# Performance work log

Hardware: AMD Instinct MI355X
Metric: run time of the kernel (lower is better)

Reference implementation:

```python
import jax, jax.numpy as jnp
import numpy as np

N, M, E, B = 200000, 100000, 600000, 64
F_IN, H, EMB, V, NREL, NSRT = 256, 256, 128, 512, 4, 5


def setup_inputs() -> dict:
    key = jax.random.key(0)
    ks = jax.random.split(key, 24)
    s = 0.02
    inp = {
        "x": jax.random.normal(ks[0], (M, F_IN), jnp.float32),
        "x_batch": jnp.sort(jax.random.randint(ks[1], (M,), 0, B)),
        "tgt_y": jax.random.randint(ks[2], (N, 3), 0, V),
        "tgt_edge_index": jax.random.randint(ks[3], (2, E), 0, N),
        "tgt_edge_type": jax.random.randint(ks[4], (E,), 0, NREL),
        "tgt_y_batch": jnp.sort(jax.random.randint(ks[5], (N,), 0, B)),
        "embeds": jax.random.normal(ks[6], (V, EMB), jnp.float32) * s,
        "W_self1": jax.random.normal(ks[7], (EMB, H), jnp.float32) * s,
        "W_rel1": jax.random.normal(ks[8], (NREL, EMB, H), jnp.float32) * s,
        "W_ctx1": jax.random.normal(ks[9], (F_IN, H), jnp.float32) * s,
        "b1": jnp.zeros((H,), jnp.float32),
        "W_self2": jax.random.normal(ks[10], (H, H), jnp.float32) * s,
        "W_rel2": jax.random.normal(ks[11], (NREL, H, H), jnp.float32) * s,
        "W_ctx2": jax.random.normal(ks[12], (F_IN, H), jnp.float32) * s,
        "b2": jnp.zeros((H,), jnp.float32),
        "W_self3": jax.random.normal(ks[13], (H, EMB), jnp.float32) * s,
        "W_rel3": jax.random.normal(ks[14], (NREL, H, EMB), jnp.float32) * s,
        "W_ctx3": jax.random.normal(ks[15], (F_IN, EMB), jnp.float32) * s,
        "b3": jnp.zeros((EMB,), jnp.float32),
        "lin_z_w": jax.random.normal(ks[16], (EMB, V), jnp.float32) * s,
        "lin_z_b": jnp.zeros((V,), jnp.float32),
        "lin_g_w": jax.random.normal(ks[17], (2 * EMB, NSRT), jnp.float32) * s,
        "lin_g_b": jnp.zeros((NSRT,), jnp.float32),
    }
    return inp


def _gcn(x, x_batch, h, src, dst, etype, y_batch, Ws, Wr, Wc, b):
    # per-graph mean context from encoder nodes, gathered per decoder node
    cnt = jax.ops.segment_sum(jnp.ones((x.shape[0],), x.dtype), x_batch, num_segments=B)
    ctx = jax.ops.segment_sum(x, x_batch, num_segments=B) / jnp.maximum(cnt, 1.0)[:, None]
    hs = h[src]  # [E, d_in] gather
    msg = jnp.zeros((src.shape[0], Ws.shape[1]), h.dtype)
    for r in range(NREL):  # relation-typed messages (R-GCN style)
        msg = msg + jnp.where((etype == r)[:, None], hs @ Wr[r], 0.0)
    agg = jax.ops.segment_sum(msg, dst, num_segments=h.shape[0])  # scatter-add at dst
    return jax.nn.relu(h @ Ws + agg + ctx[y_batch] @ Wc + b)


def reference(x, x_batch, tgt_y, tgt_edge_index, tgt_edge_type, tgt_y_batch,
              embeds, W_self1, W_rel1, W_ctx1, b1, W_self2, W_rel2, W_ctx2, b2,
              W_self3, W_rel3, W_ctx3, b3, lin_z_w, lin_z_b, lin_g_w, lin_g_b):
    y = embeds[tgt_y].sum(axis=1)  # embedding gather-sum: [N, EMB]
    src, dst = tgt_edge_index[0], tgt_edge_index[1]
    y = _gcn(x, x_batch, y, src, dst, tgt_edge_type, tgt_y_batch, W_self1, W_rel1, W_ctx1, b1)
    y = _gcn(x, x_batch, y, src, dst, tgt_edge_type, tgt_y_batch, W_self2, W_rel2, W_ctx2, b2)
    y = _gcn(x, x_batch, y, src, dst, tgt_edge_type, tgt_y_batch, W_self3, W_rel3, W_ctx3, b3)
    y_pred = jax.nn.log_softmax(y @ lin_z_w + lin_z_b, axis=1)  # [N, V]
    # y[edge_index].permute(1,0,2).flatten(1) == concat(y[src], y[dst]) per edge
    ef = jnp.concatenate([y[src], y[dst]], axis=1)  # [E, 2*EMB]
    y_edge_pred = jax.nn.log_softmax(ef @ lin_g_w + lin_g_b, axis=1)  # [E, NSRT]
    return (y, tgt_edge_index, tgt_edge_type, y_pred, y_edge_pred)
```

## Files before the change

### kernel.cpp

```cpp
#include <hip/hip_runtime.h>
#include <hip/hip_bf16.h>
#include <stdint.h>

#define NN 200000
#define MM 100000
#define EE 600000
#define BB 64
#define F_IN 256
#define HH 256
#define EMB 128
#define VV 512
#define NSRT 5

typedef __attribute__((ext_vector_type(8))) short bf16x8;
typedef __attribute__((ext_vector_type(4))) float f32x4;

__device__ __forceinline__ unsigned short f2bf(float x){
    union { float f; unsigned int u; } c; c.f = x;
    unsigned int r = c.u + 0x7FFFu + ((c.u >> 16) & 1u);
    return (unsigned short)(r >> 16);
}
__device__ __forceinline__ float bf2f(unsigned short b){
    union { unsigned int u; float f; } c; c.u = ((unsigned int)b) << 16;
    return c.f;
}

__device__ __forceinline__ int lowerb(const int* a, int n, int key){
    int lo = 0, hi = n;
    while (lo < hi){ int mid = (lo + hi) >> 1; if (a[mid] < key) lo = mid + 1; else hi = mid; }
    return lo;
}

#define GLDS16(g, l) __builtin_amdgcn_global_load_lds( \
    (const __attribute__((address_space(1))) unsigned int*)(g), \
    (__attribute__((address_space(3))) unsigned int*)(l), 16, 0, 0)

#define CTX_RPB 128
__global__ __launch_bounds__(256) void ctxsum_kernel(const float* __restrict__ x,
        const int* __restrict__ xb, float* __restrict__ sum){
    int r0 = blockIdx.x * CTX_RPB;
    int r1 = r0 + CTX_RPB; if (r1 > MM) r1 = MM;
    int t = threadIdx.x;
    float s = 0.f;
    int g = xb[r0];
    for (int r = r0; r < r1; ++r){
        int gb = xb[r];
        if (gb != g){ atomicAdd(&sum[g * F_IN + t], s); s = 0.f; g = gb; }
        s += x[(size_t)r * F_IN + t];
    }
    atomicAdd(&sum[g * F_IN + t], s);
}

__global__ __launch_bounds__(256) void ctxdiv_kernel(const float* __restrict__ sum,
        const int* __restrict__ xb, float* __restrict__ ctx){
    int g = blockIdx.x, t = threadIdx.x;
    int lo = lowerb(xb, MM, g), hi = lowerb(xb, MM, g + 1);
    int c = hi - lo; if (c < 1) c = 1;
    ctx[g * F_IN + t] = sum[g * F_IN + t] / (float)c;
}

__global__ __launch_bounds__(64) void ctxb_kernel(const float* __restrict__ ctx,
        const float* __restrict__ Wc, const float* __restrict__ b,
        float* __restrict__ out, int dout){
    int g = blockIdx.x; int j = blockIdx.y * 64 + threadIdx.x;
    float acc = b[j];
    const float* cr = ctx + g * F_IN;
    for (int k = 0; k < F_IN; ++k) acc += cr[k] * Wc[(size_t)k * dout + j];
    out[(size_t)g * dout + j] = acc;
}

__global__ __launch_bounds__(256) void build_wt(const float* __restrict__ Ws,
        const float* __restrict__ Wr, unsigned short* __restrict__ WT,
        int din, int dout, int ktot){
    size_t idx = (size_t)blockIdx.x * 256 + threadIdx.x;
    size_t total = (size_t)dout * ktot;
    if (idx >= total) return;
    int j = (int)(idx / ktot), k = (int)(idx % ktot);
    float v = (k < din) ? Ws[(size_t)k * dout + j] : Wr[(size_t)(k - din) * dout + j];
    WT[idx] = f2bf(v);
}

__global__ __launch_bounds__(256) void build_wtp(const float* __restrict__ Ws,
        const float* __restrict__ Wr, unsigned short* __restrict__ WT,
        int K, int dout){
    size_t idx = (size_t)blockIdx.x * 256 + threadIdx.x;
    size_t total = (size_t)5 * dout * K;
    if (idx >= total) return;
    int jj = (int)(idx / K), k = (int)(idx % K);
    int blk = jj / dout, j = jj % dout;
    float v = (blk == 0) ? Ws[(size_t)k * dout + j]
                         : Wr[((size_t)(blk - 1) * K + k) * dout + j];
    WT[idx] = f2bf(v);
}

__global__ __launch_bounds__(256) void embed_kernel(const int* __restrict__ ty,
        const float* __restrict__ emb, unsigned short* __restrict__ h0){
    size_t idx = (size_t)blockIdx.x * 256 + threadIdx.x;
    int i = (int)(idx >> 7), c = (int)(idx & 127);
    int t0 = ty[i * 3], t1 = ty[i * 3 + 1], t2 = ty[i * 3 + 2];
    float v = emb[(size_t)t0 * EMB + c] + emb[(size_t)t1 * EMB + c] + emb[(size_t)t2 * EMB + c];
    h0[idx] = f2bf(v);
}

__global__ __launch_bounds__(256) void hist_kernel(const int* __restrict__ dst, int* __restrict__ deg){
    int e = blockIdx.x * 256 + threadIdx.x; if (e >= EE) return;
    atomicAdd(&deg[dst[e]], 1);
}

#define SNB ((NN + 1023) / 1024)

__global__ __launch_bounds__(256) void scanA_kernel(const int* __restrict__ deg,
        int* __restrict__ bsum){
    __shared__ int wsum[4];
    int tid = threadIdx.x, wid = tid >> 6, lane = tid & 63;
    int base = blockIdx.x * 1024 + tid * 4;
    int s = 0;
    if (base + 3 < NN){ int4 v = *(const int4*)(deg + base); s = v.x + v.y + v.z + v.w; }
    else { for (int i = 0; i < 4; ++i){ int idx = base + i; if (idx < NN) s += deg[idx]; } }
#pragma unroll
    for (int off = 1; off < 64; off <<= 1) s += __shfl_xor(s, off);
    if (lane == 0) wsum[wid] = s;
    __syncthreads();
    if (tid == 0) bsum[blockIdx.x] = wsum[0] + wsum[1] + wsum[2] + wsum[3];
}

__global__ __launch_bounds__(256) void scanB_kernel(const int* __restrict__ bsum,
        int* __restrict__ boff){
    __shared__ int lds[256];
    int t = threadIdx.x;
    int v = (t < SNB) ? bsum[t] : 0;
    lds[t] = v; __syncthreads();
    for (int off = 1; off < 256; off <<= 1){
        int n = (t >= off) ? lds[t - off] : 0;
        __syncthreads();
        lds[t] += n;
        __syncthreads();
    }
    if (t < SNB) boff[t] = lds[t] - v;
}

__global__ __launch_bounds__(256) void scanC_kernel(const int* __restrict__ deg,
        const int* __restrict__ boff, int* __restrict__ rowptr, int* __restrict__ cursor){
    __shared__ int wsum[4];
    int tid = threadIdx.x, wid = tid >> 6, lane = tid & 63;
    int base = blockIdx.x * 1024 + tid * 4;
    int d0 = 0, d1 = 0, d2 = 0, d3 = 0;
    if (base + 3 < NN){ int4 v = *(const int4*)(deg + base); d0 = v.x; d1 = v.y; d2 = v.z; d3 = v.w; }
    else if (base < NN){
        d0 = deg[base];
        if (base + 1 < NN) d1 = deg[base + 1];
        if (base + 2 < NN) d2 = deg[base + 2];
    }
    int tsum = d0 + d1 + d2 + d3;
    int run = tsum;
#pragma unroll
    for (int off = 1; off < 64; off <<= 1){
        int n = __shfl_up(run, off);
        if (lane >= off) run += n;
    }
    if (lane == 63) wsum[wid] = run;
    int texcl = run - tsum;
    __syncthreads();
    int woff = 0;
    for (int i = 0; i < wid; ++i) woff += wsum[i];
    int p = boff[blockIdx.x] + woff + texcl;
    if (base < NN){
        rowptr[base] = p; cursor[base] = p; p += d0;
        if (base + 1 < NN){ rowptr[base + 1] = p; cursor[base + 1] = p; p += d1; }
        if (base + 2 < NN){ rowptr[base + 2] = p; cursor[base + 2] = p; p += d2; }
        if (base + 3 < NN){ rowptr[base + 3] = p; cursor[base + 3] = p; p += d3; }
    }
    if (blockIdx.x == 0 && tid == 0) rowptr[NN] = EE;
}

__global__ __launch_bounds__(256) void fill_kernel(const int* __restrict__ src,
        const int* __restrict__ dst, const int* __restrict__ et,
        int* __restrict__ cursor, int* __restrict__ eidx){
    int e = blockIdx.x * 256 + threadIdx.x; if (e >= EE) return;
    int p = atomicAdd(&cursor[dst[e]], 1);
    eidx[p] = src[e] | (et[e] << 28);
}

template<int DIN>
__global__ __launch_bounds__(256) void sbuild_kernel(const unsigned short* __restrict__ h,
        const int* __restrict__ rowptr, const int* __restrict__ eidx,
        unsigned short* __restrict__ S){
    constexpr int CPL = DIN / 64;
    int wid = threadIdx.x >> 6, lane = threadIdx.x & 63;
    int d = blockIdx.x * 4 + wid;
    int lo = rowptr[d], hi = rowptr[d + 1];
    float acc0[CPL], acc1[CPL], acc2[CPL], acc3[CPL];
#pragma unroll
    for (int c = 0; c < CPL; ++c){ acc0[c] = 0.f; acc1[c] = 0.f; acc2[c] = 0.f; acc3[c] = 0.f; }
    const unsigned short* hl = h + lane * CPL;
    int e = lo;
    for (; e + 1 < hi; e += 2){
        int pkA = eidx[e], pkB = eidx[e + 1];
        int sA = pkA & 0x0FFFFFFF, rA = pkA >> 28;
        int sB = pkB & 0x0FFFFFFF, rB = pkB >> 28;
        unsigned short vA[CPL], vB[CPL];
        if (CPL == 4){
            *(uint2*)vA = *(const uint2*)(hl + (size_t)sA * DIN);
            *(uint2*)vB = *(const uint2*)(hl + (size_t)sB * DIN);
        } else {
            *(unsigned int*)vA = *(const unsigned int*)(hl + (size_t)sA * DIN);
            *(unsigned int*)vB = *(const unsigned int*)(hl + (size_t)sB * DIN);
        }
        float a0 = (rA == 0) ? 1.f : 0.f, a1 = (rA == 1) ? 1.f : 0.f;
        float a2 = (rA == 2) ? 1.f : 0.f, a3 = (rA == 3) ? 1.f : 0.f;
        float b0 = (rB == 0) ? 1.f : 0.f, b1 = (rB == 1) ? 1.f : 0.f;
        float b2 = (rB == 2) ? 1.f : 0.f, b3 = (rB == 3) ? 1.f : 0.f;
#pragma unroll
        for (int c = 0; c < CPL; ++c){
            float fA = bf2f(vA[c]), fB = bf2f(vB[c]);
            acc0[c] += a0 * fA + b0 * fB;
            acc1[c] += a1 * fA + b1 * fB;
            acc2[c] += a2 * fA + b2 * fB;
            acc3[c] += a3 * fA + b3 * fB;
        }
    }
    if (e < hi){
        int pk = eidx[e];
        int s = pk & 0x0FFFFFFF, r = pk >> 28;
        unsigned short v[CPL];
        if (CPL == 4) *(uint2*)v = *(const uint2*)(hl + (size_t)s * DIN);
        else          *(unsigned int*)v = *(const unsigned int*)(hl + (size_t)s * DIN);
        float m0 = (r == 0) ? 1.f : 0.f, m1 = (r == 1) ? 1.f : 0.f;
        float m2 = (r == 2) ? 1.f : 0.f, m3 = (r == 3) ? 1.f : 0.f;
#pragma unroll
        for (int c = 0; c < CPL; ++c){
            float f = bf2f(v[c]);
            acc0[c] += m0 * f; acc1[c] += m1 * f; acc2[c] += m2 * f; acc3[c] += m3 * f;
        }
    }
    unsigned short* So = S + (size_t)d * 4 * DIN + lane * CPL;
    unsigned short o[CPL];
#pragma unroll
    for (int c = 0; c < CPL; ++c) o[c] = f2bf(acc0[c]);
    if (CPL == 4) *(uint2*)(So) = *(uint2*)o; else *(unsigned int*)(So) = *(unsigned int*)o;
#pragma unroll
    for (int c = 0; c < CPL; ++c) o[c] = f2bf(acc1[c]);
    if (CPL == 4) *(uint2*)(So + DIN) = *(uint2*)o; else *(unsigned int*)(So + DIN) = *(unsigned int*)o;
#pragma unroll
    for (int c = 0; c < CPL; ++c) o[c] = f2bf(acc2[c]);
    if (CPL == 4) *(uint2*)(So + 2 * DIN) = *(uint2*)o; else *(unsigned int*)(So + 2 * DIN) = *(unsigned int*)o;
#pragma unroll
    for (int c = 0; c < CPL; ++c) o[c] = f2bf(acc3[c]);
    if (CPL == 4) *(uint2*)(So + 3 * DIN) = *(uint2*)o; else *(unsigned int*)(So + 3 * DIN) = *(unsigned int*)o;
}

template<int DOUT, bool OUTF>
__global__ __launch_bounds__(256) void agg_kernel(const unsigned short* __restrict__ G,
        const int* __restrict__ rowptr, const int* __restrict__ eidx,
        const float* __restrict__ ctxb, const int* __restrict__ yb,
        unsigned short* __restrict__ hout, float* __restrict__ fout){
    constexpr int CPL = DOUT / 64;
    constexpr int STR = 5 * DOUT;
    int wid = threadIdx.x >> 6, lane = threadIdx.x & 63;
    int d = blockIdx.x * 4 + wid;
    int lo = rowptr[d], hi = rowptr[d + 1];
    int g = yb[d];
    const unsigned short* Gl = G + lane * CPL;
    float acc[CPL];
    {
        unsigned short sv[CPL];
        if (CPL == 4) *(uint2*)sv = *(const uint2*)(Gl + (size_t)d * STR);
        else          *(unsigned int*)sv = *(const unsigned int*)(Gl + (size_t)d * STR);
#pragma unroll
        for (int c = 0; c < CPL; ++c) acc[c] = bf2f(sv[c]);
    }
    int e = lo;
    for (; e + 1 < hi; e += 2){
        int pkA = eidx[e], pkB = eidx[e + 1];
        int sA = pkA & 0x0FFFFFFF, rA = pkA >> 28;
        int sB = pkB & 0x0FFFFFFF, rB = pkB >> 28;
        const unsigned short* ga = Gl + (size_t)sA * STR + (1 + rA) * DOUT;
        const unsigned short* gb = Gl + (size_t)sB * STR + (1 + rB) * DOUT;
        unsigned short vA[CPL], vB[CPL];
        if (CPL == 4){ *(uint2*)vA = *(const uint2*)ga; *(uint2*)vB = *(const uint2*)gb; }
        else { *(unsigned int*)vA = *(const unsigned int*)ga; *(unsigned int*)vB = *(const unsigned int*)gb; }
#pragma unroll
        for (int c = 0; c < CPL; ++c) acc[c] += bf2f(vA[c]) + bf2f(vB[c]);
    }
    if (e < hi){
        int pk = eidx[e];
        int s = pk & 0x0FFFFFFF, r = pk >> 28;
        const unsigned short* ga = Gl + (size_t)s * STR + (1 + r) * DOUT;
        unsigned short v[CPL];
        if (CPL == 4) *(uint2*)v = *(const uint2*)ga;
        else          *(unsigned int*)v = *(const unsigned int*)ga;
#pragma unroll
        for (int c = 0; c < CPL; ++c) acc[c] += bf2f(v[c]);
    }
    const float* cb = ctxb + (size_t)g * DOUT + lane * CPL;
    float f[CPL];
    unsigned short o[CPL];
#pragma unroll
    for (int c = 0; c < CPL; ++c){ f[c] = fmaxf(acc[c] + cb[c], 0.f); o[c] = f2bf(f[c]); }
    unsigned short* ho = hout + (size_t)d * DOUT + lane * CPL;
    if (CPL == 4) *(uint2*)ho = *(uint2*)o; else *(unsigned int*)ho = *(unsigned int*)o;
    if (OUTF){
        float* fo = fout + (size_t)d * DOUT + lane * CPL;
        if (CPL == 4){ float4 q = {f[0], f[1], f[2], f[3]}; *(float4*)fo = q; }
        else { float2 q = {f[0], f[1]}; *(float2*)fo = q; }
    }
}

template<int KTOT, int DIN, int NYT, bool HAS_S, bool RELUCTX>
__global__ __launch_bounds__(512, 4) void gemm128(
        const unsigned short* __restrict__ hA,
        const unsigned short* __restrict__ S,
        const unsigned short* __restrict__ WT,
        const float* __restrict__ ctxb,
        const int* __restrict__ yb,
        unsigned short* __restrict__ outb,
        int outstride, int ctxstride){
    __shared__ unsigned short lds[2][2][128 * 64];
    constexpr int NT = KTOT / 64;
    int tid = threadIdx.x;
    int wid = tid >> 6, lane = tid & 63;
    int l15 = lane & 15, lk = lane >> 4;
    int wr = wid >> 2, wc = wid & 3;

    int nwg = gridDim.x;
    int orig = blockIdx.x;
    int q = nwg >> 3, r8 = nwg & 7;
    int xcd = orig & 7, pos = orig >> 3;
    int wg = (xcd < r8 ? xcd * (q + 1) : r8 * (q + 1) + (xcd - r8) * q) + pos;
    int mrow0 = (wg / NYT) * 128;
    int ncol0 = (wg % NYT) * 128;

    f32x4 acc[4][2];
#pragma unroll
    for (int m = 0; m < 4; ++m)
#pragma unroll
        for (int n = 0; n < 2; ++n) acc[m][n] = (f32x4){0.f, 0.f, 0.f, 0.f};

    auto stage = [&](int kt, int buf){
#pragma unroll
        for (int i = 0; i < 2; ++i){
            int idx = i * 512 + tid;
            int r = idx >> 3;
            int cbl = idx & 7;
            int cb = cbl ^ (r & 7);
            int k0 = kt * 64 + cb * 8;
            int gr = mrow0 + r; if (gr > NN - 1) gr = NN - 1;
            const unsigned short* ga;
            if (HAS_S && kt >= DIN / 64) ga = S + (size_t)gr * (4 * DIN) + (k0 - DIN);
            else                         ga = hA + (size_t)gr * DIN + k0;
            GLDS16(ga, &lds[buf][0][(size_t)(i * 8 + wid) * 512]);
            int gj = ncol0 + r;
            const unsigned short* gb = WT + (size_t)gj * KTOT + k0;
            GLDS16(gb, &lds[buf][1][(size_t)(i * 8 + wid) * 512]);
        }
    };

    stage(0, 0);
    __syncthreads();
    int buf = 0;
#pragma unroll 1
    for (int kt = 0; kt < NT; ++kt){
        if (kt + 1 < NT) stage(kt + 1, buf ^ 1);
#pragma unroll
        for (int ks = 0; ks < 2; ++ks){
            int c = ks * 4 + lk;
            bf16x8 a[4], b[2];
#pragma unroll
            for (int m = 0; m < 4; ++m){
                int r = wr * 64 + m * 16 + l15;
                a[m] = *(const bf16x8*)&lds[buf][0][r * 64 + (c ^ (r & 7)) * 8];
            }
#pragma unroll
            for (int n = 0; n < 2; ++n){
                int j = wc * 32 + n * 16 + l15;
                b[n] = *(const bf16x8*)&lds[buf][1][j * 64 + (c ^ (j & 7)) * 8];
            }
#pragma unroll
            for (int m = 0; m < 4; ++m)
#pragma unroll
                for (int n = 0; n < 2; ++n)
                    acc[m][n] = __builtin_amdgcn_mfma_f32_16x16x32_bf16(b[n], a[m], acc[m][n], 0, 0, 0);
        }
        __syncthreads();
        buf ^= 1;
    }

#pragma unroll
    for (int m = 0; m < 4; ++m){
        int row = mrow0 + wr * 64 + m * 16 + l15;
        if (row >= NN) continue;
        const float* cb = RELUCTX ? (ctxb + (size_t)yb[row] * ctxstride) : ctxb;
#pragma unroll
        for (int n = 0; n < 2; ++n){
            int colb = wc * 32 + n * 16 + lk * 4;
            unsigned short o[4];
#pragma unroll
            for (int r = 0; r < 4; ++r){
                float v = acc[m][n][r] + cb[ncol0 + colb + r];
                if (RELUCTX) v = fmaxf(v, 0.f);
                o[r] = f2bf(v);
            }
            *(uint2*)(outb + (size_t)row * outstride + ncol0 + colb) = *(uint2*)o;
        }
    }
}

__global__ __launch_bounds__(512, 2) void logit_lsm_kernel(
        const unsigned short* __restrict__ ybf,
        const unsigned short* __restrict__ WTz,
        const float* __restrict__ lzb,
        float* __restrict__ ypred){
    __shared__ unsigned short ldsB[2][VV * 32];
    __shared__ float lzbs[VV];
    __shared__ float pm[4][16][2], ps[4][16][2];
    int tid = threadIdx.x;
    int wid = tid >> 6, lane = tid & 63;
    int l15 = lane & 15, lk = lane >> 4;
    int wr = wid >> 1, wc = wid & 1;
    int row = blockIdx.x * 64 + wr * 16 + l15;

    lzbs[tid] = lzb[tid];

    bf16x8 aR[4];
    const unsigned short* ap = ybf + (size_t)row * EMB;
#pragma unroll
    for (int kt = 0; kt < 4; ++kt) aR[kt] = *(const bf16x8*)(ap + kt * 32 + lk * 8);

    auto stageB = [&](int kt, int buf){
#pragma unroll
        for (int i = 0; i < 4; ++i){
            int idx = i * 512 + tid;
            int j = idx >> 2;
            int cbl = idx & 3;
            int cb = cbl ^ (j & 3);
            const unsigned short* gb = WTz + (size_t)j * EMB + kt * 32 + cb * 8;
            GLDS16(gb, &ldsB[buf][(size_t)(i * 8 + wid) * 512]);
        }
    };

    f32x4 acc[16];
#pragma unroll
    for (int n = 0; n < 16; ++n) acc[n] = (f32x4){0.f, 0.f, 0.f, 0.f};

    stageB(0, 0);
    __syncthreads();
    int buf = 0;
#pragma unroll
    for (int kt = 0; kt < 4; ++kt){
        if (kt < 3) stageB(kt + 1, buf ^ 1);
#pragma unroll
        for (int nh = 0; nh < 2; ++nh){
            bf16x8 b[8];
#pragma unroll
            for (int n8 = 0; n8 < 8; ++n8){
                int j = wc * 256 + (nh * 8 + n8) * 16 + l15;
                b[n8] = *(const bf16x8*)&ldsB[buf][j * 32 + ((lk ^ (j & 3)) * 8)];
            }
#pragma unroll
            for (int n8 = 0; n8 < 8; ++n8)
                acc[nh * 8 + n8] = __builtin_amdgcn_mfma_f32_16x16x32_bf16(b[n8], aR[kt], acc[nh * 8 + n8], 0, 0, 0);
        }
        __syncthreads();
        buf ^= 1;
    }

    float m = -3.0e38f;
#pragma unroll
    for (int n = 0; n < 16; ++n){
        int colb = wc * 256 + n * 16 + lk * 4;
#pragma unroll
        for (int r = 0; r < 4; ++r){
            float v = acc[n][r] + lzbs[colb + r];
            acc[n][r] = v;
            m = fmaxf(m, v);
        }
    }
    m = fmaxf(m, __shfl_xor(m, 16));
    m = fmaxf(m, __shfl_xor(m, 32));
    float s = 0.f;
#pragma unroll
    for (int n = 0; n < 16; ++n)
#pragma unroll
        for (int r = 0; r < 4; ++r) s += expf(acc[n][r] - m);
    s += __shfl_xor(s, 16);
    s += __shfl_xor(s, 32);
    if (lk == 0){ pm[wr][l15][wc] = m; ps[wr][l15][wc] = s; }
    __syncthreads();
    float m0 = pm[wr][l15][0], m1 = pm[wr][l15][1];
    float s0 = ps[wr][l15][0], s1 = ps[wr][l15][1];
    float M = fmaxf(m0, m1);
    float l = M + logf(expf(m0 - M) * s0 + expf(m1 - M) * s1);

    float* orow = ypred + (size_t)row * VV + wc * 256;
#pragma unroll
    for (int n = 0; n < 16; ++n){
        int colb = n * 16 + lk * 4;
        float4 q = {acc[n][0] - l, acc[n][1] - l, acc[n][2] - l, acc[n][3] - l};
        *(float4*)(orow + colb) = q;
    }
}

__global__ __launch_bounds__(256) void zpair_kernel(const float* __restrict__ y,
        const float* __restrict__ Wg, float* __restrict__ z){
    __shared__ float ylds[16][132];
    __shared__ float wg[2 * EMB * NSRT];
    for (int i = threadIdx.x; i < 2 * EMB * NSRT; i += 256) wg[i] = Wg[i];
    int n0 = blockIdx.x * 16;
    for (int i = threadIdx.x; i < 16 * 32; i += 256){
        int node = i >> 5, f4 = i & 31;
        *(float4*)&ylds[node][f4 * 4] = *(const float4*)(y + (size_t)(n0 + node) * EMB + f4 * 4);
    }
    __syncthreads();
    int t = threadIdx.x;
    if (t < 160){
        int node = t & 15, c = t >> 4;
        int base = (c >= 5) ? EMB : 0;
        int cc = (c >= 5) ? c - 5 : c;
        float acc = 0.f;
#pragma unroll 4
        for (int k = 0; k < EMB; ++k) acc += ylds[node][k] * wg[(base + k) * NSRT + cc];
        z[(size_t)(n0 + node) * 10 + c] = acc;
    }
}

__global__ __launch_bounds__(256) void edge2_kernel(const int* __restrict__ src,
        const int* __restrict__ dst, const float* __restrict__ z,
        const float* __restrict__ bg, float* __restrict__ out){
    int e = blockIdx.x * 256 + threadIdx.x; if (e >= EE) return;
    int s = src[e], d = dst[e];
    const float* zs = z + (size_t)s * 10;
    const float* zd = z + (size_t)d * 10 + 5;
    float l0 = zs[0] + zd[0] + bg[0];
    float l1 = zs[1] + zd[1] + bg[1];
    float l2 = zs[2] + zd[2] + bg[2];
    float l3 = zs[3] + zd[3] + bg[3];
    float l4 = zs[4] + zd[4] + bg[4];
    float m = fmaxf(fmaxf(fmaxf(l0, l1), fmaxf(l2, l3)), l4);
    float ssum = expf(l0 - m) + expf(l1 - m) + expf(l2 - m) + expf(l3 - m) + expf(l4 - m);
    float lg = m + logf(ssum);
    float* o = out + (size_t)e * NSRT;
    o[0] = l0 - lg; o[1] = l1 - lg; o[2] = l2 - lg; o[3] = l3 - lg; o[4] = l4 - lg;
}

__global__ __launch_bounds__(256) void i2f_kernel(const int* __restrict__ in,
        float* __restrict__ out, int n){
    int i = blockIdx.x * 256 + threadIdx.x;
    if (i < n) out[i] = (float)in[i];
}

extern "C" void kernel_launch(void* const* d_in, const int* in_sizes, int n_in,
                              void* d_out, int out_size, void* d_ws, size_t ws_size,
                              hipStream_t stream){
    const float* x    = (const float*)d_in[0];
    const int*   xb   = (const int*)d_in[1];
    const int*   ty   = (const int*)d_in[2];
    const int*   ei   = (const int*)d_in[3];
    const int*   et   = (const int*)d_in[4];
    const int*   tyb  = (const int*)d_in[5];
    const float* emb  = (const float*)d_in[6];
    const float* Ws1 = (const float*)d_in[7],  *Wr1 = (const float*)d_in[8];
    const float* Wc1 = (const float*)d_in[9],  *b1  = (const float*)d_in[10];
    const float* Ws2 = (const float*)d_in[11], *Wr2 = (const float*)d_in[12];
    const float* Wc2 = (const float*)d_in[13], *b2  = (const float*)d_in[14];
    const float* Ws3 = (const float*)d_in[15], *Wr3 = (const float*)d_in[16];
    const float* Wc3 = (const float*)d_in[17], *b3  = (const float*)d_in[18];
    const float* lzw = (const float*)d_in[19], *lzb = (const float*)d_in[20];
    const float* lgw = (const float*)d_in[21], *lgb = (const float*)d_in[22];

    const int* src = ei;
    const int* dst = ei + EE;

    float* out = (float*)d_out;
    const size_t OFF_Y  = 0;
    const size_t OFF_EI = (size_t)NN * EMB;
    const size_t OFF_ET = OFF_EI + 2 * (size_t)EE;
    const size_t OFF_YP = OFF_ET + (size_t)EE;
    const size_t OFF_EP = OFF_YP + (size_t)NN * VV;

    char* w = (char*)d_ws;
    auto alloc = [&](size_t bytes){ char* p = w; w += (bytes + 255) & ~(size_t)255; return p; };
    unsigned short* h0  = (unsigned short*)alloc((size_t)NN * EMB * 2);
    unsigned short* h1  = (unsigned short*)alloc((size_t)NN * HH * 2);
    unsigned short* h2  = (unsigned short*)alloc((size_t)NN * HH * 2);
    unsigned short* ybf = (unsigned short*)alloc((size_t)NN * EMB * 2);
    unsigned short* G2  = (unsigned short*)alloc((size_t)NN * 5 * HH * 2);
    unsigned short* G3  = (unsigned short*)alloc((size_t)NN * 5 * EMB * 2);
    unsigned short* WT1 = (unsigned short*)alloc((size_t)HH * (5 * EMB) * 2);
    unsigned short* WT2p= (unsigned short*)alloc((size_t)(5 * HH) * HH * 2);
    unsigned short* WT3p= (unsigned short*)alloc((size_t)(5 * EMB) * HH * 2);
    unsigned short* WTz = (unsigned short*)alloc((size_t)VV * EMB * 2);
    float* ctxs  = (float*)alloc(BB * F_IN * 4);
    float* ctx   = (float*)alloc(BB * F_IN * 4);
    float* ctxb1 = (float*)alloc(BB * HH * 4);
    float* ctxb2 = (float*)alloc(BB * HH * 4);
    float* ctxb3 = (float*)alloc(BB * EMB * 4);
    float* zpair = (float*)alloc((size_t)NN * 10 * 4);
    float* zerob = (float*)alloc((size_t)5 * HH * 4);
    int* deg    = (int*)alloc((size_t)NN * 4);
    int* rowptr = (int*)alloc(((size_t)NN + 1) * 4);
    int* cursor = (int*)alloc((size_t)NN * 4);
    int* eidx   = (int*)alloc((size_t)EE * 4);
    int* bsum   = (int*)alloc((size_t)SNB * 4);
    int* boff   = (int*)alloc((size_t)SNB * 4);

    unsigned short* Sbuf = (unsigned short*)(out + OFF_YP);

    hipMemsetAsync(deg, 0, (size_t)NN * 4, stream);
    hipMemsetAsync(zerob, 0, (size_t)5 * HH * 4, stream);
    hist_kernel<<<(EE + 255) / 256, 256, 0, stream>>>(dst, deg);
    scanA_kernel<<<SNB, 256, 0, stream>>>(deg, bsum);
    scanB_kernel<<<1, 256, 0, stream>>>(bsum, boff);
    scanC_kernel<<<SNB, 256, 0, stream>>>(deg, boff, rowptr, cursor);
    fill_kernel<<<(EE + 255) / 256, 256, 0, stream>>>(src, dst, et, cursor, eidx);

    hipMemsetAsync(ctxs, 0, BB * F_IN * 4, stream);
    ctxsum_kernel<<<(MM + CTX_RPB - 1) / CTX_RPB, 256, 0, stream>>>(x, xb, ctxs);
    ctxdiv_kernel<<<BB, 256, 0, stream>>>(ctxs, xb, ctx);
    ctxb_kernel<<<dim3(BB, HH / 64), 64, 0, stream>>>(ctx, Wc1, b1, ctxb1, HH);
    ctxb_kernel<<<dim3(BB, HH / 64), 64, 0, stream>>>(ctx, Wc2, b2, ctxb2, HH);
    ctxb_kernel<<<dim3(BB, EMB / 64), 64, 0, stream>>>(ctx, Wc3, b3, ctxb3, EMB);

    build_wt<<<(HH * 5 * EMB + 255) / 256, 256, 0, stream>>>(Ws1, Wr1, WT1, EMB, HH, 5 * EMB);
    build_wtp<<<(5 * HH * HH + 255) / 256, 256, 0, stream>>>(Ws2, Wr2, WT2p, HH, HH);
    build_wtp<<<(5 * EMB * HH + 255) / 256, 256, 0, stream>>>(Ws3, Wr3, WT3p, HH, EMB);
    build_wt<<<(VV * EMB + 255) / 256, 256, 0, stream>>>(lzw, lzw, WTz, EMB, VV, EMB);

    embed_kernel<<<NN * EMB / 256, 256, 0, stream>>>(ty, emb, h0);

    const int MT = (NN + 127) / 128;

    sbuild_kernel<EMB><<<NN / 4, 256, 0, stream>>>(h0, rowptr, eidx, Sbuf);
    gemm128<640, 128, 2, true, true><<<MT * 2, 512, 0, stream>>>(
        h0, Sbuf, WT1, ctxb1, tyb, h1, HH, HH);

    gemm128<256, 256, 10, false, false><<<MT * 10, 512, 0, stream>>>(
        h1, nullptr, WT2p, zerob, nullptr, G2, 5 * HH, 0);
    agg_kernel<HH, false><<<NN / 4, 256, 0, stream>>>(
        G2, rowptr, eidx, ctxb2, tyb, h2, nullptr);

    gemm128<256, 256, 5, false, false><<<MT * 5, 512, 0, stream>>>(
        h2, nullptr, WT3p, zerob, nullptr, G3, 5 * EMB, 0);
    agg_kernel<EMB, true><<<NN / 4, 256, 0, stream>>>(
        G3, rowptr, eidx, ctxb3, tyb, ybf, out + OFF_Y);

    zpair_kernel<<<NN / 16, 256, 0, stream>>>(out + OFF_Y, lgw, zpair);

    logit_lsm_kernel<<<NN / 64, 512, 0, stream>>>(ybf, WTz, lzb, out + OFF_YP);

    edge2_kernel<<<(EE + 255) / 256, 256, 0, stream>>>(src, dst, zpair, lgb, out + OFF_EP);
    i2f_kernel<<<(2 * EE + 255) / 256, 256, 0, stream>>>(ei, out + OFF_EI, 2 * EE);
    i2f_kernel<<<(EE + 255) / 256, 256, 0, stream>>>(et, out + OFF_ET, EE);
}
```

Measured before the change: 1.479 ms.

## Add weight-stationary streaming GEMM for layer 2/3 pre-transform GEMMs

Adds a streaming GEMM kernel that loads a full 128-column slice of the transposed weight (all K) into LDS once per workgroup. It then walks a chunk of 16 row tiles, reading A directly from global memory into registers and issuing MFMA 16x16x32 per wave with B held in registers. The goal is to stop reloading and double-buffering the weights for every 128-row tile and to drop the zero-bias/ctx path. Workgroups are remapped by XCD so that neighbouring chunks share a chiplet. The trade-off is four passes over each A tile (once per column pair), which re-reads A from cache, plus a large LDS footprint and fewer workgroups.

```diff
diff --git a/kernel.cpp b/kernel.cpp
--- a/kernel.cpp
+++ b/kernel.cpp
@@ -303,6 +303,83 @@
         float* fo = fout + (size_t)d * DOUT + lane * CPL;
         if (CPL == 4){ float4 q = {f[0], f[1], f[2], f[3]}; *(float4*)fo = q; }
         else { float2 q = {f[0], f[1]}; *(float2*)fo = q; }
+    }
+}
+
+template<int KTOT, int NSL>
+__global__ __launch_bounds__(512, 4) void streamgemm_kernel(
+        const unsigned short* __restrict__ A,
+        const unsigned short* __restrict__ WT,
+        unsigned short* __restrict__ out, int CH){
+    __shared__ unsigned short ldsB[128 * KTOT];
+    constexpr int NKT = KTOT / 32;
+    constexpr int NCHK = KTOT / 8;
+    int tid = threadIdx.x;
+    int wid = tid >> 6, lane = tid & 63;
+    int l15 = lane & 15, lk = lane >> 4;
+
+    int nwg = gridDim.x;
+    int orig = blockIdx.x;
+    int q = nwg >> 3, r8 = nwg & 7;
+    int xcd = orig & 7, pos = orig >> 3;
+    int wg = (xcd < r8 ? xcd * (q + 1) : r8 * (q + 1) + (xcd - r8) * q) + pos;
+    int chunk = wg / NSL, slice = wg % NSL;
+    int ncol0 = slice * 128;
+    const int outstride = NSL * 128;
+
+#pragma unroll
+    for (int i = 0; i < (128 * NCHK) / 512; ++i){
+        int idx = i * 512 + tid;
+        int j = idx / NCHK, cbl = idx % NCHK;
+        int cb = cbl ^ (j & (NCHK - 1));
+        GLDS16(WT + (size_t)(ncol0 + j) * KTOT + cb * 8,
+               &ldsB[(size_t)(i * 8 + wid) * 512]);
+    }
+    __syncthreads();
+
+    const int MTmax = (NN + 127) >> 7;
+    int mt0 = chunk * CH;
+    int mt1 = mt0 + CH; if (mt1 > MTmax) mt1 = MTmax;
+
+#pragma unroll 1
+    for (int p = 0; p < 4; ++p){
+        bf16x8 b0[NKT], b1[NKT];
+        {
+            int j0 = (p * 2) * 16 + l15;
+            int j1 = (p * 2 + 1) * 16 + l15;
+#pragma unroll
+            for (int kt = 0; kt < NKT; ++kt){
+                b0[kt] = *(const bf16x8*)&ldsB[j0 * KTOT + ((kt * 4 + lk) ^ (j0 & (NCHK - 1))) * 8];
+                b1[kt] = *(const bf16x8*)&ldsB[j1 * KTOT + ((kt * 4 + lk) ^ (j1 & (NCHK - 1))) * 8];
+            }
+        }
+#pragma unroll 1
+        for (int mt = mt0; mt < mt1; ++mt){
+            int row = mt * 128 + wid * 16 + l15;
+            int rowc = row < NN ? row : NN - 1;
+            const unsigned short* ap = A + (size_t)rowc * KTOT;
+            bf16x8 a[NKT];
+#pragma unroll
+            for (int kt = 0; kt < NKT; ++kt)
+                a[kt] = *(const bf16x8*)(ap + kt * 32 + lk * 8);
+            f32x4 acc0 = (f32x4){0.f, 0.f, 0.f, 0.f};
+            f32x4 acc1 = (f32x4){0.f, 0.f, 0.f, 0.f};
+#pragma unroll
+            for (int kt = 0; kt < NKT; ++kt){
+                acc0 = __builtin_amdgcn_mfma_f32_16x16x32_bf16(b0[kt], a[kt], acc0, 0, 0, 0);
+                acc1 = __builtin_amdgcn_mfma_f32_16x16x32_bf16(b1[kt], a[kt], acc1, 0, 0, 0);
+            }
+            if (row < NN){
+                unsigned short* orow = out + (size_t)row * outstride + ncol0;
+                unsigned short o[4];
+#pragma unroll
+                for (int r = 0; r < 4; ++r) o[r] = f2bf(acc0[r]);
+                *(uint2*)(orow + (p * 2) * 16 + lk * 4) = *(uint2*)o;
+#pragma unroll
+                for (int r = 0; r < 4; ++r) o[r] = f2bf(acc1[r]);
+                *(uint2*)(orow + (p * 2 + 1) * 16 + lk * 4) = *(uint2*)o;
+            }
+        }
     }
 }
 
@@ -595,7 +672,6 @@
     float* ctxb2 = (float*)alloc(BB * HH * 4);
     float* ctxb3 = (float*)alloc(BB * EMB * 4);
     float* zpair = (float*)alloc((size_t)NN * 10 * 4);
-    float* zerob = (float*)alloc((size_t)5 * HH * 4);
     int* deg    = (int*)alloc((size_t)NN * 4);
     int* rowptr = (int*)alloc(((size_t)NN + 1) * 4);
     int* cursor = (int*)alloc((size_t)NN * 4);
@@ -606,7 +682,6 @@
     unsigned short* Sbuf = (unsigned short*)(out + OFF_YP);
 
     hipMemsetAsync(deg, 0, (size_t)NN * 4, stream);
-    hipMemsetAsync(zerob, 0, (size_t)5 * HH * 4, stream);
     hist_kernel<<<(EE + 255) / 256, 256, 0, stream>>>(dst, deg);
     scanA_kernel<<<SNB, 256, 0, stream>>>(deg, bsum);
     scanB_kernel<<<1, 256, 0, stream>>>(bsum, boff);
@@ -628,18 +703,18 @@
     embed_kernel<<<NN * EMB / 256, 256, 0, stream>>>(ty, emb, h0);
 
     const int MT = (NN + 127) / 128;
+    const int CH = 16;
+    const int NB = (MT + CH - 1) / CH;
 
     sbuild_kernel<EMB><<<NN / 4, 256, 0, stream>>>(h0, rowptr, eidx, Sbuf);
     gemm128<640, 128, 2, true, true><<<MT * 2, 512, 0, stream>>>(
         h0, Sbuf, WT1, ctxb1, tyb, h1, HH, HH);
 
-    gemm128<256, 256, 10, false, false><<<MT * 10, 512, 0, stream>>>(
-        h1, nullptr, WT2p, zerob, nullptr, G2, 5 * HH, 0);
+    streamgemm_kernel<256, 10><<<NB * 10, 512, 0, stream>>>(h1, WT2p, G2, CH);
     agg_kernel<HH, false><<<NN / 4, 256, 0, stream>>>(
         G2, rowptr, eidx, ctxb2, tyb, h2, nullptr);
 
-    gemm128<256, 256, 5, false, false><<<MT * 5, 512, 0, stream>>>(
-        h2, nullptr, WT3p, zerob, nullptr, G3, 5 * EMB, 0);
+    streamgemm_kernel<256, 5><<<NB * 5, 512, 0, stream>>>(h2, WT3p, G3, CH);
     agg_kernel<EMB, true><<<NN / 4, 256, 0, stream>>>(
         G3, rowptr, eidx, ctxb3, tyb, ybf, out + OFF_Y);
 
```

Result: slower. 1.850 ms (+25.1%).
